# Kernel optimization log

Hardware: AMD Instinct MI355X
Metric: run time of the kernel (lower is better)

## Reference

```python
import jax, jax.numpy as jnp
import numpy as np
from jax import lax

MAX_OBJ = 100
IOU_THRES = 0.45
SCORE_THRES = 0.25
MAX_WH = 7680.0

# xywh -> xyxy conversion matrix (same as ONNX_ORT.convert_matrix)
CONVERT = jnp.array([[1, 0, 1, 0],
                     [0, 1, 0, 1],
                     [-0.5, 0, 0.5, 0],
                     [0, -0.5, 0, 0.5]], dtype=jnp.float32)


def _iou_one_vs_all(box, boxes):
    # box: [4] xyxy, boxes: [N,4] xyxy
    x1 = jnp.maximum(box[0], boxes[:, 0])
    y1 = jnp.maximum(box[1], boxes[:, 1])
    x2 = jnp.minimum(box[2], boxes[:, 2])
    y2 = jnp.minimum(box[3], boxes[:, 3])
    inter = jnp.clip(x2 - x1, 0.0) * jnp.clip(y2 - y1, 0.0)
    a = (box[2] - box[0]) * (box[3] - box[1])
    b = (boxes[:, 2] - boxes[:, 0]) * (boxes[:, 3] - boxes[:, 1])
    return inter / (a + b - inter + 1e-9)


def _nms_indices(nmsbox, max_score):
    # Greedy class-offset NMS; returns [MAX_OBJ] indices, -1 for padding.
    valid0 = max_score >= SCORE_THRES

    def step(valid, _):
        s = jnp.where(valid, max_score, -1.0)
        i = jnp.argmax(s)
        ok = s[i] >= SCORE_THRES
        iou = _iou_one_vs_all(nmsbox[i], nmsbox)
        valid = valid & (iou <= IOU_THRES)
        valid = valid.at[i].set(False)
        return valid, jnp.where(ok, i, -1)

    _, idxs = lax.scan(step, valid0, None, length=MAX_OBJ)
    return idxs


def _forward(x1, x2, num_labels1, num_labels2):
    B, N1, _ = x1.shape
    N2 = x2.shape[1]
    # pad x1 class scores with zeros for model2's labels (appended at end)
    x1p = jnp.concatenate([x1, jnp.zeros((B, N1, num_labels2), x1.dtype)], axis=2)
    # pad x2: insert zeros for model1's labels between conf and its own classes
    x2p = jnp.concatenate([x2[:, :, 0:5],
                           jnp.zeros((B, N2, num_labels1), x2.dtype),
                           x2[:, :, 5:]], axis=2)
    x = jnp.concatenate([x1p, x2p], axis=1)  # [B, N1+N2, 5+C1+C2]

    boxes = x[:, :, :4] @ CONVERT            # xywh -> xyxy, [B,N,4]
    conf = x[:, :, 4:5]
    scores = x[:, :, 5:] * conf              # [B,N,C]
    max_score = scores.max(axis=2)           # [B,N]
    cat_id = scores.argmax(axis=2)           # [B,N]
    # class-offset boxes so NMS is class-aware
    nmsbox = boxes + cat_id[..., None].astype(boxes.dtype) * MAX_WH

    idxs = jax.vmap(_nms_indices)(lax.stop_gradient(nmsbox),
                                  lax.stop_gradient(max_score))  # [B,MAX_OBJ]
    mask = idxs >= 0
    si = jnp.maximum(idxs, 0)
    sel_boxes = jnp.take_along_axis(boxes, si[..., None], axis=1)      # [B,MAX_OBJ,4]
    sel_cat = jnp.take_along_axis(cat_id, si, axis=1).astype(boxes.dtype)
    sel_score = jnp.take_along_axis(max_score, si, axis=1)

    mf = mask.astype(boxes.dtype)
    Xcol = jnp.where(mask, jnp.arange(B)[:, None], -1).astype(boxes.dtype)
    out = jnp.concatenate([Xcol[..., None],
                           sel_boxes * mf[..., None],
                           (sel_cat * mf)[..., None],
                           (sel_score * mf)[..., None]], axis=2)
    return out.reshape(B * MAX_OBJ, 7)


def setup_inputs() -> dict:
    key = jax.random.key(0)
    k1, k2 = jax.random.split(key)
    x1 = jax.random.uniform(k1, (4, 25200, 85), dtype=jnp.float32)
    x2 = jax.random.uniform(k2, (4, 25200, 25), dtype=jnp.float32)
    return {"x1": x1, "x2": x2, "num_labels1": 80, "num_labels2": 20}


def reference(x1, x2, num_labels1, num_labels2):
    return _forward(x1, x2, num_labels1, num_labels2)
```

## Files before the change

kernel.cpp:

```cpp
#include <hip/hip_runtime.h>
#include <stdint.h>

#pragma clang fp contract(off)

#define BATCH 4
#define N1 25200
#define NROW 50400
#define NCLS 100
#define TOT (BATCH*NROW)
#define CAPB 2048
#define CAPG 1152
#define SCORE_T 0.25f
#define IOU_T 0.45f
#define MAXWH 7680.0f

#define X1_SLAB 64
#define X1_SPB 394
#define X2_SLAB 256
#define X2_SPB 99

typedef unsigned long long u64;

__device__ __forceinline__ u64 pack_key(unsigned sb, int n, int cid) {
    return ((u64)sb << 32) | ((u64)(unsigned)((n ^ 0xFFFF) & 0xFFFF) << 8) | (u64)(unsigned)cid;
}

__device__ __forceinline__ bool sup_test(float inter, float sum) {
    float d = (sum - inter) + 1e-9f;
    float t1 = IOU_T * d;
    bool hi = inter > t1 * 1.00001f;
    bool lo = inter < t1 * 0.99999f;
    if (__builtin_expect(!(hi || lo), 0)) return (inter / d) > IOU_T;
    return hi;
}

__device__ __forceinline__ float rl(float v, int srcLane) {
    return __int_as_float(__builtin_amdgcn_readlane(__float_as_int(v), srcLane));
}

__device__ __forceinline__ void blk2bucket(int blk, int& b, int& c) {
    if (blk < BATCH * 20) { b = blk / 20; c = 80 + (blk - b * 20); }
    else { int z = blk - BATCH * 20; b = z / 80; c = z - b * 80; }
}

__device__ __forceinline__ int prefix_ge(const u64* list, int cnt, u64 T) {
    int lo = 0, hi = cnt;
    while (lo < hi) {
        int mid = (lo + hi) >> 1;
        if (list[mid] >= T) lo = mid + 1; else hi = mid;
    }
    return lo;
}

__device__ __forceinline__ void sort_desc(u64* sk, int L, int t) {
    bool act = (t * 8) < L;
    u64 r[8];
    if (act) {
#pragma unroll
        for (int e = 0; e < 8; ++e) r[e] = sk[t * 8 + e];
    }
    for (int k = 2; k <= L; k <<= 1) {
        for (int j = k >> 1; j > 0; j >>= 1) {
            if (j >= 512) {
                if (act) {
#pragma unroll
                    for (int e = 0; e < 8; ++e) sk[t * 8 + e] = r[e];
                }
                __syncthreads();
                if (act) {
                    bool iAmLo = (t & (j >> 3)) == 0;
                    bool descSeg = (t & (k >> 3)) == 0;
                    bool takeMax = (descSeg == iAmLo);
#pragma unroll
                    for (int e = 0; e < 8; ++e) {
                        u64 u = r[e];
                        u64 v = sk[(t * 8 + e) ^ j];
                        bool uGE = (u >= v);
                        r[e] = (takeMax == uGE) ? u : v;
                    }
                }
                __syncthreads();
            } else if (j >= 8) {
                if (act) {
                    int dt = j >> 3;
                    bool iAmLo = (t & dt) == 0;
                    bool descSeg = (t & (k >> 3)) == 0;
                    bool takeMax = (descSeg == iAmLo);
#pragma unroll
                    for (int e = 0; e < 8; ++e) {
                        u64 u = r[e];
                        u64 v = __shfl_xor(u, dt, 64);
                        bool uGE = (u >= v);
                        r[e] = (takeMax == uGE) ? u : v;
                    }
                }
            } else {
                if (act) {
#pragma unroll
                    for (int e = 0; e < 8; ++e) {
                        if (!(e & j)) {
                            int e2 = e | j;
                            bool descSeg = (k >= 8) ? ((t & (k >> 3)) == 0)
                                                    : ((e & k) == 0);
                            u64 lo = r[e], hi = r[e2];
                            bool sw = descSeg ? (lo < hi) : (lo > hi);
                            if (sw) { r[e] = hi; r[e2] = lo; }
                        }
                    }
                }
            }
        }
    }
    if (act) {
#pragma unroll
        for (int e = 0; e < 8; ++e) sk[t * 8 + e] = r[e];
    }
    __syncthreads();
}

__global__ __launch_bounds__(256) void k_rows(const float* __restrict__ x1,
                                              const float* __restrict__ x2,
                                              float4* __restrict__ boxes4,
                                              u64* __restrict__ rowKey) {
    __shared__ float4 ld4[1600];
    float* ld = (float*)ld4;
    int blk = blockIdx.x;
    int t = threadIdx.x;
    const int NX1 = BATCH * X1_SPB;
    if (blk < NX1) {
        int b = blk / X1_SPB, s = blk - b * X1_SPB;
        int r0 = s * X1_SLAB;
        int nr = min(X1_SLAB, N1 - r0);
        const float4* src = (const float4*)(x1 + ((size_t)b * N1 + r0) * 85);
        int count4 = (nr * 85) >> 2;
        for (int i = t; i < count4; i += 256) ld4[i] = src[i];
        __syncthreads();
        int row = t >> 2, sub = t & 3;
        if (row < nr) {
            const float* p = ld + row * 85;
            float conf = p[4];
            u64 key = 0ULL;
            int base = sub * 20;
            for (int c = 0; c < 20; ++c) {
                int j = base + c;
                float v = p[5 + j] * conf;
                u64 kk = ((u64)__float_as_uint(v) << 32) | (unsigned)~(unsigned)j;
                if (kk > key) key = kk;
            }
            u64 o;
            o = __shfl_xor(key, 1, 64); if (o > key) key = o;
            o = __shfl_xor(key, 2, 64); if (o > key) key = o;
            if (sub == 0) {
                float best = __uint_as_float((unsigned)(key >> 32));
                int bestj = ~(unsigned)key;
                int n = r0 + row;
                int r = b * NROW + n;
                u64 outk = 0ULL;
                if (best >= SCORE_T) {
                    float cx = p[0], cy = p[1], w = p[2], h = p[3];
                    boxes4[r] = make_float4(cx - 0.5f * w, cy - 0.5f * h,
                                            cx + 0.5f * w, cy + 0.5f * h);
                    outk = pack_key((unsigned)(key >> 32), n, bestj);
                }
                rowKey[r] = outk;
            }
        }
    } else {
        int blk2 = blk - NX1;
        int b = blk2 / X2_SPB, s = blk2 - b * X2_SPB;
        int r0 = s * X2_SLAB;
        int nr = min(X2_SLAB, N1 - r0);
        const float4* src = (const float4*)(x2 + ((size_t)b * N1 + r0) * 25);
        int count4 = (nr * 25) >> 2;
        for (int i = t; i < count4; i += 256) ld4[i] = src[i];
        __syncthreads();
        if (t < nr) {
            const float* p = ld + t * 25;
            float conf = p[4];
            float best = 0.0f; int bestj = 0;
            for (int j2 = 0; j2 < 20; ++j2) {
                float v = p[5 + j2] * conf;
                if (v > best) { best = v; bestj = 80 + j2; }
            }
            int n = N1 + r0 + t;
            int r = b * NROW + n;
            u64 outk = 0ULL;
            if (best >= SCORE_T) {
                float cx = p[0], cy = p[1], w = p[2], h = p[3];
                boxes4[r] = make_float4(cx - 0.5f * w, cy - 0.5f * h,
                                        cx + 0.5f * w, cy + 0.5f * h);
                outk = pack_key(__float_as_uint(best), n, bestj);
            }
            rowKey[r] = outk;
        }
    }
}

__global__ __launch_bounds__(256) void k_prep(const u64* __restrict__ rowKey,
                                              u64* __restrict__ skG,
                                              int* __restrict__ cntArr) {
    __shared__ u64 sk[CAPB];
    __shared__ u64 temp2[2048];
    __shared__ int wcnt[4];
    int b, c; blk2bucket(blockIdx.x, b, c);
    int bucket = b * NCLS + c;
    int t = threadIdx.x;
    int lane = t & 63, wid = t >> 6;

    int rowBase = (c >= 80) ? N1 : 0;
    const ulonglong2* rk2 = (const ulonglong2*)(rowKey + (size_t)b * NROW + rowBase);
    const int SLICE = 3150;
    u64* temp = temp2 + wid * 512;
    int wbase = 0;
    for (int i = wid * SLICE + lane; i < (wid + 1) * SLICE; i += 64) {
        ulonglong2 kk = rk2[i];
        bool m0 = (kk.x != 0ULL) && ((int)(kk.x & 0xFF) == c);
        bool m1 = (kk.y != 0ULL) && ((int)(kk.y & 0xFF) == c);
        u64 mb0 = __ballot(m0), mb1 = __ballot(m1);
        u64 below = (1ULL << lane) - 1ULL;
        if (m0) { int p = wbase + __popcll(mb0 & below); if (p < 512) temp[p] = kk.x; }
        if (m1) { int p = wbase + __popcll(mb0) + __popcll(mb1 & below); if (p < 512) temp[p] = kk.y; }
        wbase += __popcll(mb0) + __popcll(mb1);
    }
    if (lane == 0) wcnt[wid] = min(wbase, 512);
    __syncthreads();
    int w0 = wcnt[0], w1 = wcnt[1], w2 = wcnt[2], w3 = wcnt[3];
    int cnt0 = w0 + w1 + w2 + w3;
    if (cnt0 == 0) { if (t == 0) cntArr[bucket] = 0; return; }
    int myoff = (wid > 0 ? w0 : 0) + (wid > 1 ? w1 : 0) + (wid > 2 ? w2 : 0);
    int mycnt = wcnt[wid];
    for (int i = lane; i < mycnt; i += 64) sk[myoff + i] = temp[i];
    int L = 512; while (L < cnt0) L <<= 1;
    for (int i = cnt0 + t; i < L; i += 256) sk[i] = 0ULL;
    __syncthreads();

    sort_desc(sk, L, t);

    int cw = min(cnt0, CAPG);
    for (int i = t; i < cw; i += 256) skG[(size_t)bucket * CAPG + i] = sk[i];
    if (t == 0) cntArr[bucket] = cw;
}

__global__ __launch_bounds__(64) void k_greedy(const float4* __restrict__ boxes4,
                                               const u64* __restrict__ skG,
                                               const int* __restrict__ cntArr,
                                               u64* __restrict__ accKey,
                                               int* __restrict__ accCnt) {
    __shared__ float4 accQ[100];
    __shared__ float accA[100];
    int b, c; blk2bucket(blockIdx.x, b, c);
    int bucket = b * NCLS + c;
    int lane = threadIdx.x;
    int cnt0 = cntArr[bucket];
    if (cnt0 == 0) { if (lane == 0) accCnt[bucket] = 0; return; }
    const u64* skB = skG + (size_t)bucket * CAPG;
    float off = (float)c * MAXWH;
    int m = 0;
    for (int base = 0; base < cnt0 && m < 100; base += 64) {
        int j = base + lane;
        bool alive = (j < cnt0);
        float4 a = make_float4(0.f, 0.f, 0.f, 0.f);
        float aA = 0.f; u64 myKey = 0ULL;
        if (alive) {
            myKey = skB[j];
            int n = 0xFFFF ^ (int)((myKey >> 8) & 0xFFFF);
            a = boxes4[b * NROW + n];
            a.x += off; a.y += off; a.z += off; a.w += off;
            aA = (a.z - a.x) * (a.w - a.y);
        }
        int k2 = 0;
        while (k2 < m) {
            if (__ballot(alive) == 0ULL) break;
            int rem = m - k2;
            if (rem >= 8) {
#pragma unroll
                for (int u = 0; u < 8; ++u) {
                    float4 q = accQ[k2 + u];
                    float qa = accA[k2 + u];
                    float xx1 = fmaxf(a.x, q.x), yy1 = fmaxf(a.y, q.y);
                    float xx2 = fminf(a.z, q.z), yy2 = fminf(a.w, q.w);
                    float inter = fmaxf(xx2 - xx1, 0.f) * fmaxf(yy2 - yy1, 0.f);
                    alive = alive && !sup_test(inter, qa + aA);
                }
                k2 += 8;
            } else {
                for (int u = 0; u < rem; ++u) {
                    float4 q = accQ[k2 + u];
                    float qa = accA[k2 + u];
                    float xx1 = fmaxf(a.x, q.x), yy1 = fmaxf(a.y, q.y);
                    float xx2 = fminf(a.z, q.z), yy2 = fminf(a.w, q.w);
                    float inter = fmaxf(xx2 - xx1, 0.f) * fmaxf(yy2 - yy1, 0.f);
                    alive = alive && !sup_test(inter, qa + aA);
                }
                k2 = m;
            }
        }
        u64 av = __ballot(alive);
        while (av != 0ULL && m < 100) {
            int f = __builtin_ctzll(av);
            float qx = rl(a.x, f), qy = rl(a.y, f);
            float qz = rl(a.z, f), qw = rl(a.w, f);
            float qa = rl(aA, f);
            if (lane == f) {
                accQ[m] = a; accA[m] = aA;
                accKey[(size_t)bucket * 100 + m] = myKey;
                alive = false;
            }
            ++m;
            if (alive) {
                float xx1 = fmaxf(a.x, qx), yy1 = fmaxf(a.y, qy);
                float xx2 = fminf(a.z, qz), yy2 = fminf(a.w, qw);
                float inter = fmaxf(xx2 - xx1, 0.f) * fmaxf(yy2 - yy1, 0.f);
                alive = !sup_test(inter, qa + aA);
            }
            av = __ballot(alive);
        }
    }
    if (lane == 0) accCnt[bucket] = m;
}

__global__ __launch_bounds__(256) void k_merge(const float4* __restrict__ boxes4,
                                               const u64* __restrict__ accKey,
                                               const int* __restrict__ accCnt,
                                               float* __restrict__ out) {
    __shared__ u64 sk[1024];
    __shared__ u64 head[NCLS];
    __shared__ int cnts[NCLS];
    __shared__ int pc[NCLS];
    int b = blockIdx.x, t = threadIdx.x;
    const u64* base = accKey + (size_t)b * NCLS * 100;
    if (t < NCLS) {
        int cc = accCnt[b * NCLS + t];
        cnts[t] = cc;
        head[t] = (cc > 0) ? base[t * 100] : 0ULL;
    }
    __syncthreads();
    int S = 0, ne = 0; u64 mn = ~0ULL;
    for (int c = 0; c < NCLS; ++c) {
        int cc = cnts[c];
        S += cc;
        if (cc > 0) { ++ne; u64 h = head[c]; if (h < mn) mn = h; }
    }
    u64 T;
    bool bisect;
    if (S <= 900)            { T = 0ULL; bisect = false; }
    else if (ne == NCLS)     { T = mn;   bisect = false; }
    else                     { T = 0ULL; bisect = true;  }
    if (t < NCLS) pc[t] = bisect ? 0 : prefix_ge(base + t * 100, cnts[t], T);
    __syncthreads();
    int G = 0;
    for (int c = 0; c < NCLS; ++c) G += pc[c];
    if (G > 1000) bisect = true;
    if (bisect) {
        u64 lo = 0ULL, hi = ~0ULL;
        for (int it = 0; it < 64; ++it) {
            u64 mid = lo + ((hi - lo) >> 1);
            if (t < NCLS) pc[t] = prefix_ge(base + t * 100, cnts[t], mid);
            __syncthreads();
            int cnt = 0;
            for (int c = 0; c < NCLS; ++c) cnt += pc[c];
            if (cnt >= 100 && cnt <= 1000) { T = mid; G = cnt; break; }
            if (cnt < 100) hi = mid; else lo = mid;
            __syncthreads();
        }
    }
    if (t < NCLS) {
        int off = 0;
        for (int c = 0; c < t; ++c) off += pc[c];
        int p = pc[t];
        for (int j = 0; j < p; ++j) sk[off + j] = base[t * 100 + j];
    }
    for (int i = G + t; i < 1024; i += 256) sk[i] = 0ULL;
    __syncthreads();
    sort_desc(sk, 1024, t);
    if (t < 100) {
        u64 k = sk[t];
        float* o7 = out + (size_t)(b * 100 + t) * 7;
        if (k == 0ULL) {
            o7[0] = -1.0f;
            o7[1] = 0.0f; o7[2] = 0.0f; o7[3] = 0.0f;
            o7[4] = 0.0f; o7[5] = 0.0f; o7[6] = 0.0f;
        } else {
            int n = 0xFFFF ^ (int)((k >> 8) & 0xFFFF);
            int cid = (int)(k & 0xFF);
            float4 bx = boxes4[b * NROW + n];
            o7[0] = (float)b;
            o7[1] = bx.x; o7[2] = bx.y; o7[3] = bx.z; o7[4] = bx.w;
            o7[5] = (float)cid;
            o7[6] = __uint_as_float((unsigned)(k >> 32));
        }
    }
}

extern "C" void kernel_launch(void* const* d_in, const int* in_sizes, int n_in,
                              void* d_out, int out_size, void* d_ws, size_t ws_size,
                              hipStream_t stream) {
    const float* x1 = (const float*)d_in[0];
    const float* x2 = (const float*)d_in[1];
    float* out = (float*)d_out;

    float4* boxes4 = (float4*)d_ws;
    u64* rowKey = (u64*)(boxes4 + TOT);
    u64* skG    = rowKey + TOT;
    u64* accKey = skG + (size_t)BATCH * NCLS * CAPG;
    int* cntArr = (int*)(accKey + (size_t)BATCH * NCLS * 100);
    int* accCnt = cntArr + BATCH * NCLS;

    int rowBlocks = BATCH * X1_SPB + BATCH * X2_SPB;
    k_rows<<<rowBlocks, 256, 0, stream>>>(x1, x2, boxes4, rowKey);
    k_prep<<<BATCH * NCLS, 256, 0, stream>>>(rowKey, skG, cntArr);
    k_greedy<<<BATCH * NCLS, 64, 0, stream>>>(boxes4, skG, cntArr, accKey, accCnt);
    k_merge<<<BATCH, 256, 0, stream>>>(boxes4, accKey, accCnt, out);
}
```

Before: 150.5 us.

## Fuse per-class prep and greedy NMS kernels with two-pass compaction

Merges the per-bucket sort kernel and the greedy NMS kernel into one kernel, so the sorted keys never go through global memory and one launch is removed. Compaction becomes two passes, a count followed by a prefix scan and a scatter, which reads rowKey twice but drops the per-wave temp buffers and their caps. Candidate boxes are gathered in parallel by all 256 threads into shared memory before a single wave runs the greedy loop. The trade-offs are much larger LDS use per block (about 48KB), which lowers occupancy, and three idle waves during the greedy phase.

```diff
diff --git a/kernel.cpp b/kernel.cpp
--- a/kernel.cpp
+++ b/kernel.cpp
@@ -9,7 +9,6 @@
 #define NCLS 100
 #define TOT (BATCH*NROW)
 #define CAPB 2048
-#define CAPG 1152
 #define SCORE_T 0.25f
 #define IOU_T 0.45f
 #define MAXWH 7680.0f
@@ -18,6 +17,10 @@
 #define X1_SPB 394
 #define X2_SLAB 256
 #define X2_SPB 99
+
+#define NKK 12600
+#define NIT 49
+#define NTAIL 56
 
 typedef unsigned long long u64;
 
@@ -196,12 +199,15 @@
     }
 }
 
-__global__ __launch_bounds__(256) void k_prep(const u64* __restrict__ rowKey,
-                                              u64* __restrict__ skG,
-                                              int* __restrict__ cntArr) {
+__global__ __launch_bounds__(256) void k_nms(const float4* __restrict__ boxes4,
+                                             const u64* __restrict__ rowKey,
+                                             u64* __restrict__ accKey,
+                                             int* __restrict__ accCnt) {
     __shared__ u64 sk[CAPB];
-    __shared__ u64 temp2[2048];
-    __shared__ int wcnt[4];
+    __shared__ float4 cQ[CAPB];
+    __shared__ float4 accQ[100];
+    __shared__ float accA[100];
+    __shared__ int wsum[4];
     int b, c; blk2bucket(blockIdx.x, b, c);
     int bucket = b * NCLS + c;
     int t = threadIdx.x;
@@ -209,52 +215,59 @@
 
     int rowBase = (c >= 80) ? N1 : 0;
     const ulonglong2* rk2 = (const ulonglong2*)(rowKey + (size_t)b * NROW + rowBase);
-    const int SLICE = 3150;
-    u64* temp = temp2 + wid * 512;
-    int wbase = 0;
-    for (int i = wid * SLICE + lane; i < (wid + 1) * SLICE; i += 64) {
-        ulonglong2 kk = rk2[i];
-        bool m0 = (kk.x != 0ULL) && ((int)(kk.x & 0xFF) == c);
-        bool m1 = (kk.y != 0ULL) && ((int)(kk.y & 0xFF) == c);
-        u64 mb0 = __ballot(m0), mb1 = __ballot(m1);
-        u64 below = (1ULL << lane) - 1ULL;
-        if (m0) { int p = wbase + __popcll(mb0 & below); if (p < 512) temp[p] = kk.x; }
-        if (m1) { int p = wbase + __popcll(mb0) + __popcll(mb1 & below); if (p < 512) temp[p] = kk.y; }
-        wbase += __popcll(mb0) + __popcll(mb1);
-    }
-    if (lane == 0) wcnt[wid] = min(wbase, 512);
-    __syncthreads();
-    int w0 = wcnt[0], w1 = wcnt[1], w2 = wcnt[2], w3 = wcnt[3];
-    int cnt0 = w0 + w1 + w2 + w3;
-    if (cnt0 == 0) { if (t == 0) cntArr[bucket] = 0; return; }
-    int myoff = (wid > 0 ? w0 : 0) + (wid > 1 ? w1 : 0) + (wid > 2 ? w2 : 0);
-    int mycnt = wcnt[wid];
-    for (int i = lane; i < mycnt; i += 64) sk[myoff + i] = temp[i];
+
+    int cnt = 0;
+#pragma unroll 4
+    for (int it = 0; it < NIT; ++it) {
+        ulonglong2 kk = rk2[t + (it << 8)];
+        cnt += ((kk.x != 0ULL) && ((int)(kk.x & 0xFF) == c)) ? 1 : 0;
+        cnt += ((kk.y != 0ULL) && ((int)(kk.y & 0xFF) == c)) ? 1 : 0;
+    }
+    if (t < NTAIL) {
+        ulonglong2 kk = rk2[NIT * 256 + t];
+        cnt += ((kk.x != 0ULL) && ((int)(kk.x & 0xFF) == c)) ? 1 : 0;
+        cnt += ((kk.y != 0ULL) && ((int)(kk.y & 0xFF) == c)) ? 1 : 0;
+    }
+    int inc = cnt;
+    for (int o = 1; o < 64; o <<= 1) {
+        int v = __shfl_up(inc, o, 64);
+        if (lane >= o) inc += v;
+    }
+    if (lane == 63) wsum[wid] = inc;
+    __syncthreads();
+    int cnt0 = wsum[0] + wsum[1] + wsum[2] + wsum[3];
+    if (cnt0 == 0) { if (t == 0) accCnt[bucket] = 0; return; }
+    int woff = 0;
+    for (int w = 0; w < wid; ++w) woff += wsum[w];
+    int pos = woff + inc - cnt;
+    cnt0 = min(cnt0, CAPB);
+#pragma unroll 4
+    for (int it = 0; it < NIT; ++it) {
+        ulonglong2 kk = rk2[t + (it << 8)];
+        if ((kk.x != 0ULL) && ((int)(kk.x & 0xFF) == c)) { if (pos < CAPB) sk[pos] = kk.x; ++pos; }
+        if ((kk.y != 0ULL) && ((int)(kk.y & 0xFF) == c)) { if (pos < CAPB) sk[pos] = kk.y; ++pos; }
+    }
+    if (t < NTAIL) {
+        ulonglong2 kk = rk2[NIT * 256 + t];
+        if ((kk.x != 0ULL) && ((int)(kk.x & 0xFF) == c)) { if (pos < CAPB) sk[pos] = kk.x; ++pos; }
+        if ((kk.y != 0ULL) && ((int)(kk.y & 0xFF) == c)) { if (pos < CAPB) sk[pos] = kk.y; ++pos; }
+    }
     int L = 512; while (L < cnt0) L <<= 1;
     for (int i = cnt0 + t; i < L; i += 256) sk[i] = 0ULL;
     __syncthreads();
-
     sort_desc(sk, L, t);
 
-    int cw = min(cnt0, CAPG);
-    for (int i = t; i < cw; i += 256) skG[(size_t)bucket * CAPG + i] = sk[i];
-    if (t == 0) cntArr[bucket] = cw;
-}
-
-__global__ __launch_bounds__(64) void k_greedy(const float4* __restrict__ boxes4,
-                                               const u64* __restrict__ skG,
-                                               const int* __restrict__ cntArr,
-                                               u64* __restrict__ accKey,
-                                               int* __restrict__ accCnt) {
-    __shared__ float4 accQ[100];
-    __shared__ float accA[100];
-    int b, c; blk2bucket(blockIdx.x, b, c);
-    int bucket = b * NCLS + c;
-    int lane = threadIdx.x;
-    int cnt0 = cntArr[bucket];
-    if (cnt0 == 0) { if (lane == 0) accCnt[bucket] = 0; return; }
-    const u64* skB = skG + (size_t)bucket * CAPG;
     float off = (float)c * MAXWH;
+    for (int i = t; i < cnt0; i += 256) {
+        u64 k = sk[i];
+        int n = 0xFFFF ^ (int)((k >> 8) & 0xFFFF);
+        float4 v = boxes4[b * NROW + n];
+        v.x += off; v.y += off; v.z += off; v.w += off;
+        cQ[i] = v;
+    }
+    __syncthreads();
+    if (t >= 64) return;
+
     int m = 0;
     for (int base = 0; base < cnt0 && m < 100; base += 64) {
         int j = base + lane;
@@ -262,10 +275,8 @@
         float4 a = make_float4(0.f, 0.f, 0.f, 0.f);
         float aA = 0.f; u64 myKey = 0ULL;
         if (alive) {
-            myKey = skB[j];
-            int n = 0xFFFF ^ (int)((myKey >> 8) & 0xFFFF);
-            a = boxes4[b * NROW + n];
-            a.x += off; a.y += off; a.z += off; a.w += off;
+            myKey = sk[j];
+            a = cQ[j];
             aA = (a.z - a.x) * (a.w - a.y);
         }
         int k2 = 0;
@@ -401,14 +412,11 @@
 
     float4* boxes4 = (float4*)d_ws;
     u64* rowKey = (u64*)(boxes4 + TOT);
-    u64* skG    = rowKey + TOT;
-    u64* accKey = skG + (size_t)BATCH * NCLS * CAPG;
-    int* cntArr = (int*)(accKey + (size_t)BATCH * NCLS * 100);
-    int* accCnt = cntArr + BATCH * NCLS;
+    u64* accKey = rowKey + TOT;
+    int* accCnt = (int*)(accKey + (size_t)BATCH * NCLS * 100);
 
     int rowBlocks = BATCH * X1_SPB + BATCH * X2_SPB;
     k_rows<<<rowBlocks, 256, 0, stream>>>(x1, x2, boxes4, rowKey);
-    k_prep<<<BATCH * NCLS, 256, 0, stream>>>(rowKey, skG, cntArr);
-    k_greedy<<<BATCH * NCLS, 64, 0, stream>>>(boxes4, skG, cntArr, accKey, accCnt);
+    k_nms<<<BATCH * NCLS, 256, 0, stream>>>(boxes4, rowKey, accKey, accCnt);
     k_merge<<<BATCH, 256, 0, stream>>>(boxes4, accKey, accCnt, out);
 }
```

After: 148.3 us. Within noise of the previous version (-1.5%).
